# Kernel optimization log

Measured on AMD Instinct MI355X. Metric: run time of the kernel, lower is better.

The kernel has to match this reference:

```python
import jax, jax.numpy as jnp
import numpy as np

N = 100000          # num_nodes
E = 1250000         # num_edges
H = 64              # node_hidden_size
T = 2               # num_rounds


def setup_inputs() -> dict:
    key = jax.random.key(0)
    ks = jax.random.split(key, 10)
    s = 0.1  # init scale for weights
    return {
        "x": jax.random.normal(ks[0], (N, H), dtype=jnp.float32),
        "edge_index": jax.random.randint(ks[1], (2, E), 0, N, dtype=jnp.int64),
        "edge_attr": jax.random.normal(ks[2], (E, 1), dtype=jnp.float32),
        # message layers: Linear(2H+1 -> H), one per round
        "msg_W": jax.random.normal(ks[3], (T, H, 2 * H + 1), dtype=jnp.float32) * s,
        "msg_b": jax.random.normal(ks[4], (T, H), dtype=jnp.float32) * s,
        # GRUCell params, gate order (r, z, n) as in torch
        "gru_Wih": jax.random.normal(ks[5], (T, 3 * H, H), dtype=jnp.float32) * s,
        "gru_bih": jax.random.normal(ks[6], (T, 3 * H), dtype=jnp.float32) * s,
        "gru_Whh": jax.random.normal(ks[7], (T, 3 * H, H), dtype=jnp.float32) * s,
        "gru_bhh": jax.random.normal(ks[8], (T, 3 * H), dtype=jnp.float32) * s,
    }


def _gru_cell(inp, h, Wih, bih, Whh, bhh):
    # torch.nn.GRUCell math, gate order r, z, n
    gi = inp @ Wih.T + bih   # [N, 3H]
    gh = h @ Whh.T + bhh     # [N, 3H]
    i_r, i_z, i_n = jnp.split(gi, 3, axis=1)
    h_r, h_z, h_n = jnp.split(gh, 3, axis=1)
    r = jax.nn.sigmoid(i_r + h_r)
    z = jax.nn.sigmoid(i_z + h_z)
    n = jnp.tanh(i_n + r * h_n)
    return (1.0 - z) * n + z * h


def reference(x, edge_index, edge_attr, msg_W, msg_b, gru_Wih, gru_bih, gru_Whh, gru_bhh):
    row, col = edge_index[0], edge_index[1]
    num_rounds = msg_W.shape[0]
    for t in range(num_rounds):
        src = x[row]    # [E, H]
        dest = x[col]   # [E, H]
        m_input = jnp.concatenate([dest, src, edge_attr], axis=1)  # [E, 2H+1]
        messages = m_input @ msg_W[t].T + msg_b[t]                 # [E, H]
        agg = jax.ops.segment_sum(messages, row, num_segments=x.shape[0])  # [N, H]
        x = _gru_cell(agg, x, gru_Wih[t], gru_bih[t], gru_Whh[t], gru_bhh[t])
    return x
```

## Files before the change

### kernel.cpp

```cpp
#include <hip/hip_runtime.h>
#include <hip/hip_bf16.h>
#include <hip/hip_fp16.h>

#define H 64
#define CAP 48

typedef __attribute__((ext_vector_type(8))) short short8;
typedef __attribute__((ext_vector_type(4))) float float4v;

__device__ __forceinline__ float lane_bcast(float v, int k) {
    return __int_as_float(__builtin_amdgcn_readlane(__float_as_int(v), k));
}
__device__ __forceinline__ short f2bf_bits(float f) {
    union { __hip_bfloat16 b; short s; } u;
    u.b = __float2bfloat16(f);
    return u.s;
}
__device__ __forceinline__ float bf2f(unsigned short s) {
    union { unsigned int u; float f; } v;
    v.u = ((unsigned int)s) << 16;
    return v.f;
}
__device__ __forceinline__ void split8(const float* __restrict__ p,
                                       short8& hi, short8& lo) {
    float4v f0 = *(const float4v*)p;
    float4v f1 = *(const float4v*)(p + 4);
#pragma unroll
    for (int j = 0; j < 8; j++) {
        float f = (j < 4) ? f0[j] : f1[j - 4];
        short h = f2bf_bits(f);
        float fh = bf2f((unsigned short)h);
        hi[j] = h;
        lo[j] = f2bf_bits(f - fh);
    }
}
__device__ __forceinline__ void zero8(short8& hi, short8& lo) {
#pragma unroll
    for (int j = 0; j < 8; j++) { hi[j] = 0; lo[j] = 0; }
}

#define MFMA(a, b, c) __builtin_amdgcn_mfma_f32_16x16x32_bf16(a, b, c, 0, 0, 0)

__global__ __launch_bounds__(64) void prep_msg(
    const float* __restrict__ msg_W, short* __restrict__ frag)
{
    const int slot = blockIdx.x & 15, t = blockIdx.x >> 4, lane = threadIdx.x;
    const int tile = slot >> 1, ks = slot & 1;
    const float* W = msg_W + (size_t)t * H * 129;
    const int wrow = (tile & 3) * 16 + (lane & 15);
    const int coff = (tile < 4) ? 0 : 64;
    const int kq = (lane >> 4) * 8;
    short8 hi, lo;
    split8(W + (size_t)wrow * 129 + coff + ks * 32 + kq, hi, lo);
    short8* out = (short8*)(frag + (size_t)t * 16384);
    out[slot * 64 + lane] = hi;
    out[16 * 64 + slot * 64 + lane] = lo;
}

__global__ __launch_bounds__(64) void prep_gru(
    const float* __restrict__ Wih, const float* __restrict__ Whh,
    short* __restrict__ frag)
{
    const int slot = blockIdx.x % 48, t = blockIdx.x / 48, lane = threadIdx.x;
    const int tile = slot >> 1, ks = slot & 1;
    const int kq = (lane >> 4) * 8;
    const float* Wp = (tile < 12)
        ? (Wih + (size_t)t * 192 * H + ((size_t)(tile * 16 + (lane & 15))) * H)
        : (Whh + (size_t)t * 192 * H + ((size_t)((tile - 12) * 16 + (lane & 15))) * H);
    short8 hi, lo;
    split8(Wp + ks * 32 + kq, hi, lo);
    short8* out = (short8*)(frag + (size_t)t * 49152);
    out[slot * 64 + lane] = hi;
    out[48 * 64 + slot * 64 + lane] = lo;
}

__global__ __launch_bounds__(256) void count_scatter_cast(
    const int* __restrict__ row, const int* __restrict__ col,
    const float* __restrict__ attr,
    int* __restrict__ deg, int2* __restrict__ edata,
    int E, int EB,
    const float* __restrict__ x_in, float* __restrict__ x,
    __half* __restrict__ xh, int NH8)
{
    if ((int)blockIdx.x < EB) {
        int e = blockIdx.x * 256 + threadIdx.x;
        if (e < E) {
            int r = row[e];
            int pos = atomicAdd(&deg[r], 1);
            if (pos < CAP) {
                int2 v;
                v.x = col[e];
                v.y = __float_as_int(attr[e]);
                edata[(size_t)r * CAP + pos] = v;
            }
        }
    } else {
        int i = (blockIdx.x - EB) * 256 + threadIdx.x;
        if (i < NH8) {
            const float* p = x_in + (size_t)i * 8;
            float4v f0 = *(const float4v*)p;
            float4v f1 = *(const float4v*)(p + 4);
            *(float4v*)(x + (size_t)i * 8) = f0;
            *(float4v*)(x + (size_t)i * 8 + 4) = f1;
            short8 hv;
#pragma unroll
            for (int u = 0; u < 8; u++) {
                float f = (u < 4) ? f0[u] : f1[u - 4];
                hv[u] = __half_as_short(__float2half(f));
            }
            *(short8*)(xh + (size_t)i * 8) = hv;
        }
    }
}

__global__ __launch_bounds__(256) void aggregate(
    const int* __restrict__ deg, const int2* __restrict__ edata,
    const __half* __restrict__ xh,
    float* __restrict__ s, float2* __restrict__ asum2, int N)
{
    const int tid = threadIdx.x, lane = tid & 63, wv = tid >> 6;
    const int n = blockIdx.x * 4 + wv;
    if (n >= N) return;
    int cnt = deg[n];
    if (cnt > CAP) cnt = CAP;
    int2 ed = make_int2(0, 0);
    if (lane < cnt) ed = edata[(size_t)n * CAP + lane];
    float acc0 = 0.f, acc1 = 0.f, acc2 = 0.f, acc3 = 0.f, aacc = 0.f;
    for (int j = 0; j < cnt; j += 8) {
        float v[8];
#pragma unroll
        for (int u = 0; u < 8; u++) {
            int c = __builtin_amdgcn_readlane(ed.x, j + u);
            v[u] = __half2float(xh[(size_t)c * H + lane]);
        }
#pragma unroll
        for (int u = 0; u < 8; u++) {
            float a = lane_bcast(__int_as_float(ed.y), j + u);
            aacc += a;
            float t = (j + u < cnt) ? v[u] : 0.f;
            if ((u & 3) == 0) acc0 += t;
            else if ((u & 3) == 1) acc1 += t;
            else if ((u & 3) == 2) acc2 += t;
            else acc3 += t;
        }
    }
    s[(size_t)n * H + lane] = (acc0 + acc1) + (acc2 + acc3);
    if (lane == 0) asum2[n] = make_float2(aacc, (float)cnt);
}

#define FSLOT(mt, ks, arr, hl) (((((mt) * 2 + (ks)) * 2 + (arr)) * 2 + (hl)))
__global__ __launch_bounds__(256) void fused_msg_gru(
    const float* __restrict__ s, const float2* __restrict__ asum2,
    float* __restrict__ x, __half* __restrict__ xh,
    const short* __restrict__ mfrag, const short* __restrict__ gfrag,
    const float* __restrict__ Wt, const float* __restrict__ mb,
    const float* __restrict__ bih, const float* __restrict__ bhh, int N)
{
    __shared__ short8 afrag[32 * 64];
    const int tid = threadIdx.x, lane = tid & 63, q = tid >> 6;
    const int base = blockIdx.x * 64;
    const int arow = lane & 15;
    const int kq = (lane >> 4) * 8;
    const short8* mhi = (const short8*)mfrag;
    const short8* mlo = mhi + 16 * 64;
    const short8* ghi = (const short8*)gfrag;
    const short8* glo = ghi + 48 * 64;

    {
        const int m = base + q * 16 + arow;
#pragma unroll
        for (int ks = 0; ks < 2; ks++) {
            short8 hi, lo;
            if (m < N) split8(s + (size_t)m * H + ks * 32 + kq, hi, lo);
            else       zero8(hi, lo);
            afrag[FSLOT(q, ks, 0, 0) * 64 + lane] = hi;
            afrag[FSLOT(q, ks, 0, 1) * 64 + lane] = lo;
            if (m < N) split8(x + (size_t)m * H + ks * 32 + kq, hi, lo);
            else       zero8(hi, lo);
            afrag[FSLOT(q, ks, 1, 0) * 64 + lane] = hi;
            afrag[FSLOT(q, ks, 1, 1) * 64 + lane] = lo;
        }
    }
    __syncthreads();

    float4v accd[4], accs[4];
#pragma unroll
    for (int mt = 0; mt < 4; mt++) {
        accd[mt] = (float4v){0.f, 0.f, 0.f, 0.f};
        accs[mt] = (float4v){0.f, 0.f, 0.f, 0.f};
    }
#pragma unroll
    for (int ks = 0; ks < 2; ks++) {
        short8 ah[4], al[4];
#pragma unroll
        for (int mt = 0; mt < 4; mt++) {
            ah[mt] = afrag[FSLOT(mt, ks, 0, 0) * 64 + lane];
            al[mt] = afrag[FSLOT(mt, ks, 0, 1) * 64 + lane];
        }
        const int sd = q * 2 + ks;
        short8 bh = mhi[sd * 64 + lane];
        short8 bl = mlo[sd * 64 + lane];
#pragma unroll
        for (int mt = 0; mt < 4; mt++) {
            accd[mt] = MFMA(ah[mt], bh, accd[mt]);
            accd[mt] = MFMA(al[mt], bh, accd[mt]);
            accd[mt] = MFMA(ah[mt], bl, accd[mt]);
        }
#pragma unroll
        for (int mt = 0; mt < 4; mt++) {
            ah[mt] = afrag[FSLOT(mt, ks, 1, 0) * 64 + lane];
            al[mt] = afrag[FSLOT(mt, ks, 1, 1) * 64 + lane];
        }
        const int ss = (4 + q) * 2 + ks;
        short8 ch = mhi[ss * 64 + lane];
        short8 cl = mlo[ss * 64 + lane];
#pragma unroll
        for (int mt = 0; mt < 4; mt++) {
            accs[mt] = MFMA(ah[mt], ch, accs[mt]);
            accs[mt] = MFMA(al[mt], ch, accs[mt]);
            accs[mt] = MFMA(ah[mt], cl, accs[mt]);
        }
    }

    const int colb = lane & 15;
    const int rq4 = (lane >> 4) * 4;
    const int j = q * 16 + colb;
    const int ksW  = q >> 1;
    const int quad = (j >> 3) & 3;
    const int elem = j & 7;
    float vv[4][4];
    {
        const float bj = mb[j];
        const float wa = Wt[(size_t)j * 129 + 128];
#pragma unroll
        for (int mt = 0; mt < 4; mt++) {
#pragma unroll
            for (int r = 0; r < 4; r++) {
                const int m = base + mt * 16 + rq4 + r;
                float v = 0.f;
                if (m < N) {
                    float2 da = asum2[m];
                    v = accd[mt][r] + da.y * (accs[mt][r] + bj) + wa * da.x;
                }
                vv[mt][r] = v;
            }
        }
    }
    __syncthreads();

    {
        short* af = (short*)afrag;
#pragma unroll
        for (int mt = 0; mt < 4; mt++) {
#pragma unroll
            for (int r = 0; r < 4; r++) {
                float v = vv[mt][r];
                short hi = f2bf_bits(v);
                float fh = bf2f((unsigned short)hi);
                short lo = f2bf_bits(v - fh);
                const int lane2 = (rq4 + r) | (quad << 4);
                af[(FSLOT(mt, ksW, 0, 0) * 64 + lane2) * 8 + elem] = hi;
                af[(FSLOT(mt, ksW, 0, 1) * 64 + lane2) * 8 + elem] = lo;
            }
        }
    }
    __syncthreads();

    float4v acc[6][4];
#pragma unroll
    for (int g = 0; g < 6; g++)
#pragma unroll
        for (int mt = 0; mt < 4; mt++) acc[g][mt] = (float4v){0.f, 0.f, 0.f, 0.f};

#pragma unroll
    for (int ks = 0; ks < 2; ks++) {
        short8 ah[4], al[4];
#pragma unroll
        for (int mt = 0; mt < 4; mt++) {
            ah[mt] = afrag[FSLOT(mt, ks, 0, 0) * 64 + lane];
            al[mt] = afrag[FSLOT(mt, ks, 0, 1) * 64 + lane];
        }
#pragma unroll
        for (int g = 0; g < 3; g++) {
            const int si = (g * 4 + q) * 2 + ks;
            short8 bh = ghi[si * 64 + lane];
            short8 bl = glo[si * 64 + lane];
#pragma unroll
            for (int mt = 0; mt < 4; mt++) {
                acc[g][mt] = MFMA(ah[mt], bh, acc[g][mt]);
                acc[g][mt] = MFMA(al[mt], bh, acc[g][mt]);
                acc[g][mt] = MFMA(ah[mt], bl, acc[g][mt]);
            }
        }
#pragma unroll
        for (int mt = 0; mt < 4; mt++) {
            ah[mt] = afrag[FSLOT(mt, ks, 1, 0) * 64 + lane];
            al[mt] = afrag[FSLOT(mt, ks, 1, 1) * 64 + lane];
        }
#pragma unroll
        for (int g = 0; g < 3; g++) {
            const int sh = (12 + g * 4 + q) * 2 + ks;
            short8 bh = ghi[sh * 64 + lane];
            short8 bl = glo[sh * 64 + lane];
#pragma unroll
            for (int mt = 0; mt < 4; mt++) {
                acc[3 + g][mt] = MFMA(ah[mt], bh, acc[3 + g][mt]);
                acc[3 + g][mt] = MFMA(al[mt], bh, acc[3 + g][mt]);
                acc[3 + g][mt] = MFMA(ah[mt], bl, acc[3 + g][mt]);
            }
        }
    }

    const float b_ir = bih[j], b_iz = bih[64 + j], b_in = bih[128 + j];
    const float b_hr = bhh[j], b_hz = bhh[64 + j], b_hn = bhh[128 + j];
    const short* af = (const short*)afrag;
#pragma unroll
    for (int mt = 0; mt < 4; mt++) {
#pragma unroll
        for (int r = 0; r < 4; r++) {
            const int m = base + mt * 16 + rq4 + r;
            if (m >= N) continue;
            float ir = acc[0][mt][r] + b_ir;
            float iz = acc[1][mt][r] + b_iz;
            float in_ = acc[2][mt][r] + b_in;
            float hr = acc[3][mt][r] + b_hr;
            float hz = acc[4][mt][r] + b_hz;
            float hn = acc[5][mt][r] + b_hn;
            float rr = 1.f / (1.f + __expf(-(ir + hr)));
            float zz = 1.f / (1.f + __expf(-(iz + hz)));
            float e2 = __expf(2.f * (in_ + rr * hn));
            float nn = 1.f - 2.f / (e2 + 1.f);
            const int lane2 = (rq4 + r) | (quad << 4);
            float hold = bf2f((unsigned short)af[(FSLOT(mt, ksW, 1, 0) * 64 + lane2) * 8 + elem])
                       + bf2f((unsigned short)af[(FSLOT(mt, ksW, 1, 1) * 64 + lane2) * 8 + elem]);
            float out = (1.f - zz) * nn + zz * hold;
            x[(size_t)m * H + j] = out;
            xh[(size_t)m * H + j] = __float2half(out);
        }
    }
}

extern "C" void kernel_launch(void* const* d_in, const int* in_sizes, int n_in,
                              void* d_out, int out_size, void* d_ws, size_t ws_size,
                              hipStream_t stream) {
    const float* x_in  = (const float*)d_in[0];
    const int*   ei    = (const int*)d_in[1];
    const float* attr  = (const float*)d_in[2];
    const float* msg_W = (const float*)d_in[3];
    const float* msg_b = (const float*)d_in[4];
    const float* Wih   = (const float*)d_in[5];
    const float* bih   = (const float*)d_in[6];
    const float* Whh   = (const float*)d_in[7];
    const float* bhh   = (const float*)d_in[8];

    const int N = in_sizes[0] / H;
    const int E = in_sizes[2];
    const int T = in_sizes[4] / H;
    const int* row = ei;
    const int* col = ei + E;

    float*  x       = (float*)d_out;
    float*  s       = (float*)d_ws;
    __half* xh      = (__half*)(s + (size_t)N * H);
    float2* asum2   = (float2*)(xh + (size_t)N * H);
    int*    deg     = (int*)(asum2 + N);
    int2*   edata   = (int2*)(deg + N);
    short*  msgfrag = (short*)(edata + (size_t)N * CAP);
    short*  grufrag = msgfrag + (size_t)T * 16384;

    const int eb  = (E + 255) / 256;
    const int nh8 = (N * H) / 8;
    const int cb  = (nh8 + 255) / 256;

    hipMemsetAsync(deg, 0, (size_t)N * sizeof(int), stream);

    prep_msg<<<T * 16, 64, 0, stream>>>(msg_W, msgfrag);
    prep_gru<<<T * 48, 64, 0, stream>>>(Wih, Whh, grufrag);

    count_scatter_cast<<<eb + cb, 256, 0, stream>>>(
        row, col, attr, deg, edata, E, eb, x_in, x, xh, nh8);

    const int nbq        = (N + 63) / 64;
    const int agg_blocks = (N + 3) / 4;

    for (int t = 0; t < T; t++) {
        aggregate<<<agg_blocks, 256, 0, stream>>>(deg, edata, xh, s, asum2, N);
        fused_msg_gru<<<nbq, 256, 0, stream>>>(
            s, asum2, x, xh,
            msgfrag + (size_t)t * 16384, grufrag + (size_t)t * 49152,
            msg_W + (size_t)t * H * (2 * H + 1), msg_b + (size_t)t * H,
            bih + (size_t)t * 3 * H, bhh + (size_t)t * 3 * H, N);
    }
}
```

Measured before the change: 381.9 us.

## Vectorize gather, emit bf16 split sums, separate scatter pass, drop redundant copies

The aggregate kernel now has 8 lane groups each gather a full 16-byte half row per neighbor, then reduces across groups with shuffles, instead of one scalar half load per lane per neighbor. It writes the neighbor sum directly as bf16 hi/lo pairs, so the fused kernel no longer has to split fp32 sums. The edge bucketing is split into an atomic count pass that records positions and a separate scatter pass. The initial x copy and the final xh write are dropped by reading x_in in the first round. The cost is an extra kernel launch and an extra per-edge position array, which reuses the s_lo buffer.

```diff
diff --git a/kernel.cpp b/kernel.cpp
--- a/kernel.cpp
+++ b/kernel.cpp
@@ -8,9 +8,6 @@
 typedef __attribute__((ext_vector_type(8))) short short8;
 typedef __attribute__((ext_vector_type(4))) float float4v;
 
-__device__ __forceinline__ float lane_bcast(float v, int k) {
-    return __int_as_float(__builtin_amdgcn_readlane(__float_as_int(v), k));
-}
 __device__ __forceinline__ short f2bf_bits(float f) {
     union { __hip_bfloat16 b; short s; } u;
     u.b = __float2bfloat16(f);
@@ -74,34 +71,20 @@
     out[48 * 64 + slot * 64 + lane] = lo;
 }
 
-__global__ __launch_bounds__(256) void count_scatter_cast(
-    const int* __restrict__ row, const int* __restrict__ col,
-    const float* __restrict__ attr,
-    int* __restrict__ deg, int2* __restrict__ edata,
+__global__ __launch_bounds__(256) void count_cast(
+    const int* __restrict__ row, int* __restrict__ deg, int* __restrict__ lpos,
     int E, int EB,
-    const float* __restrict__ x_in, float* __restrict__ x,
-    __half* __restrict__ xh, int NH8)
+    const float* __restrict__ x_in, __half* __restrict__ xh, int NH8)
 {
     if ((int)blockIdx.x < EB) {
         int e = blockIdx.x * 256 + threadIdx.x;
-        if (e < E) {
-            int r = row[e];
-            int pos = atomicAdd(&deg[r], 1);
-            if (pos < CAP) {
-                int2 v;
-                v.x = col[e];
-                v.y = __float_as_int(attr[e]);
-                edata[(size_t)r * CAP + pos] = v;
-            }
-        }
+        if (e < E) lpos[e] = atomicAdd(&deg[row[e]], 1);
     } else {
         int i = (blockIdx.x - EB) * 256 + threadIdx.x;
         if (i < NH8) {
             const float* p = x_in + (size_t)i * 8;
             float4v f0 = *(const float4v*)p;
             float4v f1 = *(const float4v*)(p + 4);
-            *(float4v*)(x + (size_t)i * 8) = f0;
-            *(float4v*)(x + (size_t)i * 8 + 4) = f1;
             short8 hv;
 #pragma unroll
             for (int u = 0; u < 8; u++) {
@@ -113,10 +96,28 @@
     }
 }
 
+__global__ __launch_bounds__(256) void scatter_bucket(
+    const int* __restrict__ row, const int* __restrict__ col,
+    const float* __restrict__ attr, const int* __restrict__ lpos,
+    int2* __restrict__ edata, int E)
+{
+    int e = blockIdx.x * 256 + threadIdx.x;
+    if (e < E) {
+        int p = lpos[e];
+        if (p < CAP) {
+            int2 v;
+            v.x = col[e];
+            v.y = __float_as_int(attr[e]);
+            edata[(size_t)row[e] * CAP + p] = v;
+        }
+    }
+}
+
 __global__ __launch_bounds__(256) void aggregate(
     const int* __restrict__ deg, const int2* __restrict__ edata,
     const __half* __restrict__ xh,
-    float* __restrict__ s, float2* __restrict__ asum2, int N)
+    short* __restrict__ s_hi, short* __restrict__ s_lo,
+    float2* __restrict__ asum2, int N)
 {
     const int tid = threadIdx.x, lane = tid & 63, wv = tid >> 6;
     const int n = blockIdx.x * 4 + wv;
@@ -125,36 +126,53 @@
     if (cnt > CAP) cnt = CAP;
     int2 ed = make_int2(0, 0);
     if (lane < cnt) ed = edata[(size_t)n * CAP + lane];
-    float acc0 = 0.f, acc1 = 0.f, acc2 = 0.f, acc3 = 0.f, aacc = 0.f;
+    const int g = lane >> 3;
+    const int cl = lane & 7;
+    float acc[8] = {0.f, 0.f, 0.f, 0.f, 0.f, 0.f, 0.f, 0.f};
+    float aacc = 0.f;
     for (int j = 0; j < cnt; j += 8) {
-        float v[8];
+        const int idx = j + g;
+        int   c = __shfl(ed.x, idx, 64);
+        float a = __shfl(__int_as_float(ed.y), idx, 64);
+        short8 hv = *(const short8*)(xh + (size_t)c * H + cl * 8);
+        if (idx < cnt) {
+            aacc += a;
+#pragma unroll
+            for (int u = 0; u < 8; u++)
+                acc[u] += __half2float(__ushort_as_half((unsigned short)hv[u]));
+        }
+    }
+#pragma unroll
+    for (int off = 8; off < 64; off <<= 1) {
+        aacc += __shfl_xor(aacc, off, 64);
+#pragma unroll
+        for (int u = 0; u < 8; u++) acc[u] += __shfl_xor(acc[u], off, 64);
+    }
+    if (lane < 8) {
+        short8 hi8, lo8;
 #pragma unroll
         for (int u = 0; u < 8; u++) {
-            int c = __builtin_amdgcn_readlane(ed.x, j + u);
-            v[u] = __half2float(xh[(size_t)c * H + lane]);
-        }
-#pragma unroll
-        for (int u = 0; u < 8; u++) {
-            float a = lane_bcast(__int_as_float(ed.y), j + u);
-            aacc += a;
-            float t = (j + u < cnt) ? v[u] : 0.f;
-            if ((u & 3) == 0) acc0 += t;
-            else if ((u & 3) == 1) acc1 += t;
-            else if ((u & 3) == 2) acc2 += t;
-            else acc3 += t;
-        }
-    }
-    s[(size_t)n * H + lane] = (acc0 + acc1) + (acc2 + acc3);
+            float v = acc[u];
+            short h = f2bf_bits(v);
+            hi8[u] = h;
+            lo8[u] = f2bf_bits(v - bf2f((unsigned short)h));
+        }
+        *(short8*)(s_hi + (size_t)n * H + lane * 8) = hi8;
+        *(short8*)(s_lo + (size_t)n * H + lane * 8) = lo8;
+    }
     if (lane == 0) asum2[n] = make_float2(aacc, (float)cnt);
 }
 
 #define FSLOT(mt, ks, arr, hl) (((((mt) * 2 + (ks)) * 2 + (arr)) * 2 + (hl)))
 __global__ __launch_bounds__(256) void fused_msg_gru(
-    const float* __restrict__ s, const float2* __restrict__ asum2,
+    const short* __restrict__ s_hi, const short* __restrict__ s_lo,
+    const float2* __restrict__ asum2,
+    const float* __restrict__ xf,
     float* __restrict__ x, __half* __restrict__ xh,
     const short* __restrict__ mfrag, const short* __restrict__ gfrag,
     const float* __restrict__ Wt, const float* __restrict__ mb,
-    const float* __restrict__ bih, const float* __restrict__ bhh, int N)
+    const float* __restrict__ bih, const float* __restrict__ bhh,
+    int N, int write_xh)
 {
     __shared__ short8 afrag[32 * 64];
     const int tid = threadIdx.x, lane = tid & 63, q = tid >> 6;
@@ -171,11 +189,13 @@
 #pragma unroll
         for (int ks = 0; ks < 2; ks++) {
             short8 hi, lo;
-            if (m < N) split8(s + (size_t)m * H + ks * 32 + kq, hi, lo);
-            else       zero8(hi, lo);
+            if (m < N) {
+                hi = *(const short8*)(s_hi + (size_t)m * H + ks * 32 + kq);
+                lo = *(const short8*)(s_lo + (size_t)m * H + ks * 32 + kq);
+            } else zero8(hi, lo);
             afrag[FSLOT(q, ks, 0, 0) * 64 + lane] = hi;
             afrag[FSLOT(q, ks, 0, 1) * 64 + lane] = lo;
-            if (m < N) split8(x + (size_t)m * H + ks * 32 + kq, hi, lo);
+            if (m < N) split8(xf + (size_t)m * H + ks * 32 + kq, hi, lo);
             else       zero8(hi, lo);
             afrag[FSLOT(q, ks, 1, 0) * 64 + lane] = hi;
             afrag[FSLOT(q, ks, 1, 1) * 64 + lane] = lo;
@@ -335,7 +355,7 @@
                        + bf2f((unsigned short)af[(FSLOT(mt, ksW, 1, 1) * 64 + lane2) * 8 + elem]);
             float out = (1.f - zz) * nn + zz * hold;
             x[(size_t)m * H + j] = out;
-            xh[(size_t)m * H + j] = __float2half(out);
+            if (write_xh) xh[(size_t)m * H + j] = __float2half(out);
         }
     }
 }
@@ -360,8 +380,10 @@
     const int* col = ei + E;
 
     float*  x       = (float*)d_out;
-    float*  s       = (float*)d_ws;
-    __half* xh      = (__half*)(s + (size_t)N * H);
+    short*  s_hi    = (short*)d_ws;
+    short*  s_lo    = s_hi + (size_t)N * H;
+    int*    lpos    = (int*)s_lo;
+    __half* xh      = (__half*)(s_lo + (size_t)N * H);
     float2* asum2   = (float2*)(xh + (size_t)N * H);
     int*    deg     = (int*)(asum2 + N);
     int2*   edata   = (int2*)(deg + N);
@@ -377,18 +399,21 @@
     prep_msg<<<T * 16, 64, 0, stream>>>(msg_W, msgfrag);
     prep_gru<<<T * 48, 64, 0, stream>>>(Wih, Whh, grufrag);
 
-    count_scatter_cast<<<eb + cb, 256, 0, stream>>>(
-        row, col, attr, deg, edata, E, eb, x_in, x, xh, nh8);
+    count_cast<<<eb + cb, 256, 0, stream>>>(row, deg, lpos, E, eb, x_in, xh, nh8);
+    scatter_bucket<<<eb, 256, 0, stream>>>(row, col, attr, lpos, edata, E);
 
     const int nbq        = (N + 63) / 64;
     const int agg_blocks = (N + 3) / 4;
 
     for (int t = 0; t < T; t++) {
-        aggregate<<<agg_blocks, 256, 0, stream>>>(deg, edata, xh, s, asum2, N);
+        aggregate<<<agg_blocks, 256, 0, stream>>>(
+            deg, edata, xh, s_hi, s_lo, asum2, N);
         fused_msg_gru<<<nbq, 256, 0, stream>>>(
-            s, asum2, x, xh,
+            s_hi, s_lo, asum2,
+            (t == 0) ? x_in : x, x, xh,
             msgfrag + (size_t)t * 16384, grufrag + (size_t)t * 49152,
             msg_W + (size_t)t * H * (2 * H + 1), msg_b + (size_t)t * H,
-            bih + (size_t)t * 3 * H, bhh + (size_t)t * 3 * H, N);
-    }
-}
+            bih + (size_t)t * 3 * H, bhh + (size_t)t * 3 * H,
+            N, (t + 1 < T) ? 1 : 0);
+    }
+}
```

Result: faster. 361.5 us (-5.3%).
